# Performance work log

Hardware: AMD Instinct MI355X
Metric: run time of the kernel (lower is better)

Reference implementation:

```python
import jax, jax.numpy as jnp
import numpy as np

B, V = 16, 262144

def _make_T():
    # 16x9 spherical-harmonics -> 4x4 irradiance transform matrix (Ramamoorthi & Hanrahan)
    c = np.array([0.429043, 0.511664, 0.743125, 0.886227, 0.247708])
    rows = np.array(list(range(16)) + [15])
    cols = np.array([8, 4, 7, 3, 4, 8, 5, 1, 7, 5, 6, 2, 3, 1, 2, 0, 6])
    vals = np.array([c[0], c[0], c[0], c[1],
                     c[0], -c[0], c[0], c[1],
                     c[0], c[0], c[2], c[1],
                     c[1], c[1], c[1], c[3], -c[4]])
    T = np.zeros((16, 9), dtype=np.float32)
    T[rows, cols] = vals  # no duplicate (row, col) pairs
    return jnp.asarray(T)


def setup_inputs() -> dict:
    key = jax.random.key(0)
    k1, k2, k3 = jax.random.split(key, 3)
    light = jax.random.normal(k1, (3,), dtype=jnp.float32)
    normals = jax.random.normal(k2, (B, V, 3), dtype=jnp.float32)
    sh_coeffs = jax.random.normal(k3, (27,), dtype=jnp.float32)  # 9 SH coeffs per RGB channel
    return {"light": light, "normals": normals, "sh_coeffs": sh_coeffs}


def reference(light, normals, sh_coeffs):
    b, v = normals.shape[0], normals.shape[1]
    # augment normals with homogeneous 1 -> [B, V, 4]
    N = jnp.concatenate([normals, jnp.ones((b, v, 1), dtype=normals.dtype)], axis=2)
    T = _make_T()
    # per-channel 4x4 transform: M[c] = (T @ sh9_c).reshape(4, 4)
    M = (T @ sh_coeffs.reshape(3, 9).T).T.reshape(3, 4, 4)  # [3, 4, 4]
    # MN[c, b] = M[c] @ N[b].T  -> [3, B, 4, V]
    MN = jnp.einsum('cij,bvj->cbiv', M, N)
    # faithful to torch: MN[c,b] (shape [4,V]) is row-major .view()'d to [V,4]
    MNr = MN.reshape(3, b, v, 4)
    # per-vertex dot product, stacked over RGB -> [B, V, 3]
    E_rgb = jnp.einsum('bvj,cbvj->bvc', N, MNr)
    return E_rgb
```

## Files before the change

kernel.cpp:

```cpp
#include <hip/hip_runtime.h>


#define SH_V 262144
#define SH_B 16
#define QTR  65536

__global__ __launch_bounds__(256, 8) void sh_lighting_kernel(
    const float* __restrict__ normals,
    const float* __restrict__ sh,
    float* __restrict__ out)
{
    __shared__ float nbr[3072];

    const int tid  = threadIdx.x;
    const int lane = tid & 63;
    const int w    = tid >> 6;
    const int blk  = blockIdx.x;
    const int b    = blk >> 8;
    const int ublk = blk & 255;
    const int u0   = ublk << 8;
    const int nb0  = u0 << 2;

    const float* nbase = normals + (size_t)b * (SH_V * 3);

    {
        const float* src = nbase + (size_t)nb0 * 3;
#pragma unroll
        for (int k = 0; k < 3; ++k) {
            const int idx = 192 * w + 64 * k + lane;
            __builtin_amdgcn_global_load_lds(
                (const __attribute__((address_space(1))) void*)(src + (size_t)idx * 4),
                (__attribute__((address_space(3))) void*)(&nbr[idx * 4]),
                16, 0, 0);
        }
    }

    float3 own[4];
#pragma unroll
    for (int m = 0; m < 4; ++m) {
        own[m] = *(const float3*)(nbase + (size_t)(u0 + tid + m * QTR) * 3);
    }

    const float c0 = 0.429043f, c1 = 0.511664f, c2 = 0.743125f,
                c3 = 0.886227f, c4 = 0.247708f;
    float M[3][4][4];
#pragma unroll
    for (int c = 0; c < 3; ++c) {
        const float L0 = sh[9*c+0], L1 = sh[9*c+1], L2 = sh[9*c+2];
        const float L3 = sh[9*c+3], L4 = sh[9*c+4], L5 = sh[9*c+5];
        const float L6 = sh[9*c+6], L7 = sh[9*c+7], L8 = sh[9*c+8];
        M[c][0][0] = c0*L8;  M[c][0][1] = c0*L4;  M[c][0][2] = c0*L7;  M[c][0][3] = c1*L3;
        M[c][1][0] = c0*L4;  M[c][1][1] = -c0*L8; M[c][1][2] = c0*L5;  M[c][1][3] = c1*L1;
        M[c][2][0] = c0*L7;  M[c][2][1] = c0*L5;  M[c][2][2] = c2*L6;  M[c][2][3] = c1*L2;
        M[c][3][0] = c1*L3;  M[c][3][1] = c1*L1;  M[c][3][2] = c1*L2;  M[c][3][3] = c3*L0 - c4*L6;
    }

    asm volatile("s_waitcnt vmcnt(0)" ::: "memory");
    __builtin_amdgcn_sched_barrier(0);

    const float4* lp = (const float4*)(&nbr[12 * tid]);
    const float4 q0 = lp[0], q1 = lp[1], q2 = lp[2];
    const float ng[12] = {q0.x,q0.y,q0.z,q0.w, q1.x,q1.y,q1.z,q1.w, q2.x,q2.y,q2.z,q2.w};

    float* obase = out + (size_t)b * (SH_V * 3);

#pragma unroll
    for (int m = 0; m < 4; ++m) {
        const float nx = own[m].x, ny = own[m].y, nz = own[m].z;
        const float dx = fmaf(nx, ng[0], fmaf(ny, ng[3], fmaf(nz, ng[6], ng[9])));
        const float dy = fmaf(nx, ng[1], fmaf(ny, ng[4], fmaf(nz, ng[7], ng[10])));
        const float dz = fmaf(nx, ng[2], fmaf(ny, ng[5], fmaf(nz, ng[8], ng[11])));
        const float dw = nx + ny + nz + 1.0f;

        float* op = obase + (size_t)(u0 + tid + m * QTR) * 3;
        __builtin_nontemporal_store(
            fmaf(M[0][m][0], dx, fmaf(M[0][m][1], dy, fmaf(M[0][m][2], dz, M[0][m][3] * dw))), op);
        __builtin_nontemporal_store(
            fmaf(M[1][m][0], dx, fmaf(M[1][m][1], dy, fmaf(M[1][m][2], dz, M[1][m][3] * dw))), op + 1);
        __builtin_nontemporal_store(
            fmaf(M[2][m][0], dx, fmaf(M[2][m][1], dy, fmaf(M[2][m][2], dz, M[2][m][3] * dw))), op + 2);
    }
}

extern "C" void kernel_launch(void* const* d_in, const int* in_sizes, int n_in,
                              void* d_out, int out_size, void* d_ws, size_t ws_size,
                              hipStream_t stream) {
    const float* normals = (const float*)d_in[1];
    const float* sh      = (const float*)d_in[2];
    float* out           = (float*)d_out;

    const int grid = SH_B * (QTR / 256);
    sh_lighting_kernel<<<grid, 256, 0, stream>>>(normals, sh, out);
}
```

Before: 26.33 us.

## Stage own-normal loads and outputs through LDS for 16-byte coalesced access

Per-thread float3 global loads of the four own vertices become direct 16-byte global-to-LDS loads into a shared buffer. The three scalar strided nontemporal stores per vertex are replaced by writes to an LDS result tile, followed by coalesced 16-byte vector nontemporal stores. LDS use per block triples and __syncthreads barriers are added, so the occupancy hint drops from 8 to 4 blocks. The aim is fewer, wider memory transactions in a bandwidth-bound kernel, paid for with extra LDS traffic and barrier stalls.

```diff
diff --git a/kernel.cpp b/kernel.cpp
--- a/kernel.cpp
+++ b/kernel.cpp
@@ -5,12 +5,16 @@
 #define SH_B 16
 #define QTR  65536
 
-__global__ __launch_bounds__(256, 8) void sh_lighting_kernel(
+typedef float f32x4 __attribute__((ext_vector_type(4)));
+
+__global__ __launch_bounds__(256, 4) void sh_lighting_kernel(
     const float* __restrict__ normals,
     const float* __restrict__ sh,
     float* __restrict__ out)
 {
-    __shared__ float nbr[3072];
+    __shared__ float nbr [3072];
+    __shared__ float ownb[3072];
+    __shared__ float res [3072];
 
     const int tid  = threadIdx.x;
     const int lane = tid & 63;
@@ -27,7 +31,7 @@
         const float* src = nbase + (size_t)nb0 * 3;
 #pragma unroll
         for (int k = 0; k < 3; ++k) {
-            const int idx = 192 * w + 64 * k + lane;
+            const int idx = k * 256 + tid;
             __builtin_amdgcn_global_load_lds(
                 (const __attribute__((address_space(1))) void*)(src + (size_t)idx * 4),
                 (__attribute__((address_space(3))) void*)(&nbr[idx * 4]),
@@ -35,10 +39,18 @@
         }
     }
 
-    float3 own[4];
+    {
 #pragma unroll
-    for (int m = 0; m < 4; ++m) {
-        own[m] = *(const float3*)(nbase + (size_t)(u0 + tid + m * QTR) * 3);
+        for (int k = 0; k < 3; ++k) {
+            const int g = k * 256 + tid;
+            const int m = g / 192;
+            const int j = g - m * 192;
+            const float* src = nbase + ((size_t)(u0 + m * QTR) * 3 + (size_t)j * 4);
+            __builtin_amdgcn_global_load_lds(
+                (const __attribute__((address_space(1))) void*)src,
+                (__attribute__((address_space(3))) void*)(&ownb[g * 4]),
+                16, 0, 0);
+        }
     }
 
     const float c0 = 0.429043f, c1 = 0.511664f, c2 = 0.743125f,
@@ -55,30 +67,41 @@
         M[c][3][0] = c1*L3;  M[c][3][1] = c1*L1;  M[c][3][2] = c1*L2;  M[c][3][3] = c3*L0 - c4*L6;
     }
 
-    asm volatile("s_waitcnt vmcnt(0)" ::: "memory");
-    __builtin_amdgcn_sched_barrier(0);
+    __syncthreads();
 
-    const float4* lp = (const float4*)(&nbr[12 * tid]);
-    const float4 q0 = lp[0], q1 = lp[1], q2 = lp[2];
+    const f32x4* lp = (const f32x4*)(&nbr[12 * tid]);
+    const f32x4 q0 = lp[0], q1 = lp[1], q2 = lp[2];
     const float ng[12] = {q0.x,q0.y,q0.z,q0.w, q1.x,q1.y,q1.z,q1.w, q2.x,q2.y,q2.z,q2.w};
-
-    float* obase = out + (size_t)b * (SH_V * 3);
 
 #pragma unroll
     for (int m = 0; m < 4; ++m) {
-        const float nx = own[m].x, ny = own[m].y, nz = own[m].z;
+        const float nx = ownb[m*768 + 3*tid + 0];
+        const float ny = ownb[m*768 + 3*tid + 1];
+        const float nz = ownb[m*768 + 3*tid + 2];
         const float dx = fmaf(nx, ng[0], fmaf(ny, ng[3], fmaf(nz, ng[6], ng[9])));
         const float dy = fmaf(nx, ng[1], fmaf(ny, ng[4], fmaf(nz, ng[7], ng[10])));
         const float dz = fmaf(nx, ng[2], fmaf(ny, ng[5], fmaf(nz, ng[8], ng[11])));
         const float dw = nx + ny + nz + 1.0f;
 
-        float* op = obase + (size_t)(u0 + tid + m * QTR) * 3;
-        __builtin_nontemporal_store(
-            fmaf(M[0][m][0], dx, fmaf(M[0][m][1], dy, fmaf(M[0][m][2], dz, M[0][m][3] * dw))), op);
-        __builtin_nontemporal_store(
-            fmaf(M[1][m][0], dx, fmaf(M[1][m][1], dy, fmaf(M[1][m][2], dz, M[1][m][3] * dw))), op + 1);
-        __builtin_nontemporal_store(
-            fmaf(M[2][m][0], dx, fmaf(M[2][m][1], dy, fmaf(M[2][m][2], dz, M[2][m][3] * dw))), op + 2);
+        res[m*768 + 3*tid + 0] =
+            fmaf(M[0][m][0], dx, fmaf(M[0][m][1], dy, fmaf(M[0][m][2], dz, M[0][m][3] * dw)));
+        res[m*768 + 3*tid + 1] =
+            fmaf(M[1][m][0], dx, fmaf(M[1][m][1], dy, fmaf(M[1][m][2], dz, M[1][m][3] * dw)));
+        res[m*768 + 3*tid + 2] =
+            fmaf(M[2][m][0], dx, fmaf(M[2][m][1], dy, fmaf(M[2][m][2], dz, M[2][m][3] * dw)));
+    }
+
+    __syncthreads();
+
+    {
+        float* obase = out + (size_t)b * (SH_V * 3) + (size_t)(u0 + w * QTR) * 3;
+        const f32x4* rp = (const f32x4*)(&res[w * 768]);
+#pragma unroll
+        for (int k = 0; k < 3; ++k) {
+            const int j = k * 64 + lane;
+            const f32x4 val = rp[j];
+            __builtin_nontemporal_store(val, (f32x4*)(obase + (size_t)j * 4));
+        }
     }
 }
 
```

Result: no change. 25.93 us (-1.5%).
